# Kernel tuning notes

Hardware: AMD Instinct MI355X
Metric: run time of the kernel (lower is better)

The kernel has to match this reference:

```python
import jax, jax.numpy as jnp
import numpy as np

GAMMA = 2.0
EPS = 1e-12  # tf.nn.l2_normalize epsilon


def setup_inputs() -> dict:
    key = jax.random.key(0)
    k1, k2 = jax.random.split(key)
    B, H, W_, C = 8, 56, 56, 256
    x = jax.random.normal(k1, (B, H, W_, C), dtype=jnp.float32)
    W = jax.random.normal(k2, (C, C), dtype=jnp.float32) * 0.05
    return {"x": x, "W": W}


def reference(x, W):
    B, H, Wd, C = x.shape
    hw = H * Wd
    # transform branch: 1x1 conv, no bias (num_layers=1)
    t = jnp.einsum('bhwc,cd->bhwd', x, W).reshape(B, hw, C)
    # pixel affinity: cosine similarity (tf: -cosine_similarity == cos sim)
    xf = x.reshape(B, hw, C)
    inv_norm = jax.lax.rsqrt(jnp.maximum(jnp.sum(xf * xf, axis=-1, keepdims=True), EPS))
    xn = xf * inv_norm
    sim = jnp.einsum('bic,bjc->bij', xn, xn)  # [B, hw, hw]
    sim = jnp.power(jax.nn.relu(sim), GAMMA)
    y = jnp.einsum('bij,bjc->bic', sim, t)
    return y.reshape(B, H, Wd, C)
```

## Files before the change

kernel.cpp:

```cpp
#include <hip/hip_runtime.h>

#define HW 3136
#define CH 256
#define NJT 49
#define NIT 25
#define NPIX 25088

typedef __attribute__((ext_vector_type(8))) short bf16x8;
typedef __attribute__((ext_vector_type(4))) float f32x4;
typedef __attribute__((ext_vector_type(16))) float f32x16;
typedef unsigned short u16;
typedef unsigned int u32;

static __device__ __forceinline__ u16 f2bf(float f){
  union { float f; u32 u; } v; v.f = f;
  u32 r = v.u + 0x7FFFu + ((v.u >> 16) & 1u);
  return (u16)(r >> 16);
}

static __device__ __forceinline__ void gload16(const void* g, void* l){
  __builtin_amdgcn_global_load_lds(
      (const __attribute__((address_space(1))) unsigned int*)g,
      (__attribute__((address_space(3))) unsigned int*)l, 16, 0, 0);
}

static __device__ __forceinline__ f32x16 zero16(){
  f32x16 v;
  #pragma unroll
  for (int e = 0; e < 16; ++e) v[e] = 0.f;
  return v;
}

#define MFMA32(A,B,C) __builtin_amdgcn_mfma_f32_32x32x16_bf16((A),(B),(C),0,0,0)

__global__ __launch_bounds__(256) void prep_wt(const float* __restrict__ W,
                                               u16* __restrict__ Wt){
  const int o = blockIdx.x, i = threadIdx.x;
  Wt[o*CH + i] = f2bf(W[i*CH + o]);
}

__global__ __launch_bounds__(256) void gemm_t(const float* __restrict__ x,
                                              const u16* __restrict__ Wt,
                                              u16* __restrict__ xn_bf,
                                              u16* __restrict__ tT){
  __shared__ u16 sT[256*64];
  const int jt = blockIdx.x, b = blockIdx.y;
  const int tid = threadIdx.x, wid = tid >> 6, lane = tid & 63;
  const int l15 = lane & 15, l4 = lane >> 4;
  const int j0 = jt * 64;
  const int row = j0 + wid*16 + l15;
  const float* xp = x + ((size_t)b*HW + row)*CH + l4*8;

  float xv[8][8];
  float ss = 0.f;
  #pragma unroll
  for (int kb = 0; kb < 8; ++kb){
    const float4 v0 = *(const float4*)(xp + kb*32);
    const float4 v1 = *(const float4*)(xp + kb*32 + 4);
    xv[kb][0]=v0.x; xv[kb][1]=v0.y; xv[kb][2]=v0.z; xv[kb][3]=v0.w;
    xv[kb][4]=v1.x; xv[kb][5]=v1.y; xv[kb][6]=v1.z; xv[kb][7]=v1.w;
    #pragma unroll
    for (int e = 0; e < 8; ++e) ss += xv[kb][e]*xv[kb][e];
  }
  ss += __shfl_xor(ss, 16);
  ss += __shfl_xor(ss, 32);
  const float inv = rsqrtf(fmaxf(ss, 1e-12f));

  bf16x8 ax[8];
  #pragma unroll
  for (int kb = 0; kb < 8; ++kb){
    bf16x8 a, n;
    #pragma unroll
    for (int e = 0; e < 8; ++e){
      a[e] = (short)f2bf(xv[kb][e]);
      n[e] = (short)f2bf(xv[kb][e]*inv);
    }
    ax[kb] = a;
    *(bf16x8*)(xn_bf + ((size_t)b*HW + row)*CH + kb*32 + l4*8) = n;
  }

  f32x4 acc[16];
  #pragma unroll
  for (int n = 0; n < 16; ++n) acc[n] = f32x4{0.f,0.f,0.f,0.f};
  #pragma unroll
  for (int kb = 0; kb < 8; ++kb){
    #pragma unroll
    for (int n0 = 0; n0 < 16; ++n0){
      const bf16x8 bb = *(const bf16x8*)(Wt + (n0*16 + l15)*CH + kb*32 + l4*8);
      acc[n0] = __builtin_amdgcn_mfma_f32_16x16x32_bf16(ax[kb], bb, acc[n0], 0, 0, 0);
    }
  }
  #pragma unroll
  for (int n0 = 0; n0 < 16; ++n0){
    const int c = n0*16 + l15;
    const int jloc = wid*16 + l4*4;
    const int gj = jloc >> 3;
    ushort4 w4;
    w4.x = f2bf(acc[n0][0]); w4.y = f2bf(acc[n0][1]);
    w4.z = f2bf(acc[n0][2]); w4.w = f2bf(acc[n0][3]);
    *(ushort4*)&sT[c*64 + ((gj ^ (c & 7)) * 8) + (jloc & 7)] = w4;
  }
  __syncthreads();
  #pragma unroll
  for (int p = 0; p < 8; ++p){
    const int c = p*32 + (tid >> 3);
    const int q = tid & 7;
    const bf16x8 v = *(const bf16x8*)&sT[c*64 + ((q ^ (c & 7)) * 8)];
    *(bf16x8*)(tT + ((size_t)b*CH + c)*HW + j0 + q*8) = v;
  }
}

__global__ __launch_bounds__(512) void ppm_main(const u16* __restrict__ xn,
                                                const u16* __restrict__ tT,
                                                float* __restrict__ out){
  __shared__ u16 SM[73728];

  const int it = blockIdx.x, b = blockIdx.y;
  const int tid = threadIdx.x, wid = tid >> 6, lane = tid & 63;
  const int l31 = lane & 31, hi = lane >> 5;
  const int i0 = it * 128;
  const int wj = wid >> 2, wi = wid & 3;
  u16* sPB = SM + 65536;

  bf16x8 aq[16];
  {
    int irow = i0 + wi*32 + l31;
    if (irow >= HW) irow = HW - 1;
    const u16* p = xn + ((size_t)b*HW + irow)*CH + hi*8;
    #pragma unroll
    for (int ks = 0; ks < 16; ++ks) aq[ks] = *(const bf16x8*)(p + ks*16);
  }

  f32x16 accY[4];
  #pragma unroll
  for (int cb = 0; cb < 4; ++cb) accY[cb] = zero16();

  const size_t xbase = (size_t)b*HW;
  const size_t tbase = (size_t)b*CH;

  {
    u16* nXJ = SM;
    u16* nTJ = SM + 16384;
    #pragma unroll
    for (int q = 0; q < 4; ++q){
      const int m = q*512 + tid;
      { const int row = m >> 5, g = m & 31;
        gload16(xn + (xbase + row)*CH + ((g ^ (row & 7))*8), &nXJ[m*8]); }
      { const int c = m >> 3, g = m & 7;
        gload16(tT + (tbase + c)*HW + ((g ^ (c & 7))*8), &nTJ[m*8]); }
    }
    __syncthreads();
  }

  #pragma unroll 1
  for (int jt = 0; jt < NJT; ++jt){
    const int buf = jt & 1;
    u16* sXJ = SM + buf*32768;
    u16* sTJ = sXJ + 16384;

    if (jt + 1 < NJT){
      u16* nXJ = SM + (buf ^ 1)*32768;
      u16* nTJ = nXJ + 16384;
      const int j0n = (jt + 1)*64;
      #pragma unroll
      for (int q = 0; q < 4; ++q){
        const int m = q*512 + tid;
        { const int row = m >> 5, g = m & 31;
          gload16(xn + (xbase + j0n + row)*CH + ((g ^ (row & 7))*8), &nXJ[m*8]); }
        { const int c = m >> 3, g = m & 7;
          gload16(tT + (tbase + c)*HW + j0n + ((g ^ (c & 7))*8), &nTJ[m*8]); }
      }
    }

    f32x16 sa = zero16(), sb = zero16();
    const int rj = wj*32 + l31;
    const int rsw = rj & 7;
    const u16* xjrow = &sXJ[rj*256];
    __builtin_amdgcn_s_setprio(1);
    #pragma unroll
    for (int kb = 0; kb < 8; ++kb){
      const bf16x8 a0 = *(const bf16x8*)&xjrow[(((kb*4 + hi)     ^ rsw) * 8)];
      const bf16x8 a1 = *(const bf16x8*)&xjrow[(((kb*4 + 2 + hi) ^ rsw) * 8)];
      sa = MFMA32(a0, aq[2*kb],   sa);
      sb = MFMA32(a1, aq[2*kb+1], sb);
    }
    __builtin_amdgcn_s_setprio(0);

    float s0,s1,s2,s3,s4,s5,s6,s7,s8,s9,s10,s11,s12,s13,s14,s15;
#define SREL(d, r) { float v_ = sa[r] + sb[r]; v_ = fmaxf(v_, 0.f); d = v_ * v_; }
    SREL(s0,0) SREL(s1,1) SREL(s2,2) SREL(s3,3) SREL(s4,4) SREL(s5,5) SREL(s6,6) SREL(s7,7)
    SREL(s8,8) SREL(s9,9) SREL(s10,10) SREL(s11,11) SREL(s12,12) SREL(s13,13) SREL(s14,14) SREL(s15,15)
#undef SREL
    u32 w0,w1,w2,w3,w4,w5,w6,w7;
#define PK(d, a, c) asm("v_cvt_pk_bf16_f32 %0, %1, %2" : "=v"(d) : "v"(a), "v"(c));
    PK(w0, s0, s1)  PK(w1, s2, s3)  PK(w2, s4, s5)  PK(w3, s6, s7)
    PK(w4, s8, s9)  PK(w5, s10,s11) PK(w6, s12,s13) PK(w7, s14,s15)
#undef PK
    asm volatile("v_permlane32_swap_b32 %0, %1" : "+v"(w0), "+v"(w2));
    asm volatile("v_permlane32_swap_b32 %0, %1" : "+v"(w1), "+v"(w3));
    asm volatile("v_permlane32_swap_b32 %0, %1" : "+v"(w4), "+v"(w6));
    asm volatile("v_permlane32_swap_b32 %0, %1" : "+v"(w5), "+v"(w7));
    union { u32 u[4]; bf16x8 v; } fb0, fb1;
    fb0.u[0]=w0; fb0.u[1]=w1; fb0.u[2]=w2; fb0.u[3]=w3;
    fb1.u[0]=w4; fb1.u[1]=w5; fb1.u[2]=w6; fb1.u[3]=w7;

    *(bf16x8*)&sPB[(wi*4 + 2*wj + 0)*512 + lane*8] = fb0.v;
    *(bf16x8*)&sPB[(wi*4 + 2*wj + 1)*512 + lane*8] = fb1.v;
    __syncthreads();

    bf16x8 pb[4];
    #pragma unroll
    for (int ks = 0; ks < 4; ++ks)
      pb[ks] = *(const bf16x8*)&sPB[(wi*4 + ks)*512 + lane*8];

    __builtin_amdgcn_s_setprio(1);
    #pragma unroll
    for (int ks = 0; ks < 4; ++ks){
      #pragma unroll
      for (int cb = 0; cb < 4; ++cb){
        const int c = wj*128 + cb*32 + l31;
        const bf16x8 af = *(const bf16x8*)&sTJ[c*64 + (((ks*2 + hi) ^ (c & 7)) * 8)];
        accY[cb] = MFMA32(af, pb[ks], accY[cb]);
      }
    }
    __builtin_amdgcn_s_setprio(0);

    __syncthreads();
  }

  float* Yl = (float*)SM;
  {
    const int il = wi*32 + l31;
    const int isw = (il & 7) << 2;
    #pragma unroll
    for (int cb = 0; cb < 4; ++cb)
      #pragma unroll
      for (int r = 0; r < 16; ++r){
        const int c = wj*128 + cb*32 + (r & 3) + 8*(r >> 2) + 4*hi;
        Yl[il*256 + (c ^ isw)] = accY[cb][r];
      }
  }
  __syncthreads();
  {
    const int i3 = tid >> 2;
    const int cq = (tid & 3) * 64;
    const int sw3 = (i3 & 7) << 2;
    if (i0 + i3 < HW){
      float* orow = out + ((size_t)b*HW + i0 + i3)*CH;
      #pragma unroll
      for (int q = 0; q < 16; ++q){
        const int c = cq + q*4;
        const float4 v = *(const float4*)&Yl[i3*256 + (c ^ sw3)];
        *(float4*)&orow[c] = v;
      }
    }
  }
}

extern "C" void kernel_launch(void* const* d_in, const int* in_sizes, int n_in,
                              void* d_out, int out_size, void* d_ws, size_t ws_size,
                              hipStream_t stream){
  const float* x = (const float*)d_in[0];
  const float* W = (const float*)d_in[1];
  float* out = (float*)d_out;
  char* ws = (char*)d_ws;

  const size_t SZ = (size_t)NPIX * CH * sizeof(u16);
  u16* xn_bf = (u16*)(ws);
  u16* tT    = (u16*)(ws + SZ);
  u16* Wt    = (u16*)(ws + 2*SZ);

  prep_wt<<<CH, CH, 0, stream>>>(W, Wt);
  gemm_t<<<dim3(NJT, 8), 256, 0, stream>>>(x, Wt, xn_bf, tT);
  ppm_main<<<dim3(NIT, 8), 512, 0, stream>>>(xn_bf, tT, out);
}
```

Measured before the change: 149.8 us.

## Software-pipeline the P·T MFMA stage one tile behind the similarity stage

The loop is restructured so that the second GEMM (similarity tile times transformed features) for tile jt-1 runs in the same iteration as the first GEMM for tile jt. The X and T tile loads are split into separate double-buffered stages, and the P buffer is double-buffered too. This removes one __syncthreads per iteration and lets the two MFMA phases and the loads interleave. In exchange, LDS use grows from 144 KiB to 160 KiB per block, which leaves no LDS headroom, and a final drain PV step is added after the loop.

Result: no change. 150.3 us (+0.3%).

```diff
diff --git a/kernel.cpp b/kernel.cpp
--- a/kernel.cpp
+++ b/kernel.cpp
@@ -113,14 +113,13 @@
 __global__ __launch_bounds__(512) void ppm_main(const u16* __restrict__ xn,
                                                 const u16* __restrict__ tT,
                                                 float* __restrict__ out){
-  __shared__ u16 SM[73728];
+  __shared__ u16 SM[81920];
 
   const int it = blockIdx.x, b = blockIdx.y;
   const int tid = threadIdx.x, wid = tid >> 6, lane = tid & 63;
   const int l31 = lane & 31, hi = lane >> 5;
   const int i0 = it * 128;
   const int wj = wid >> 2, wi = wid & 3;
-  u16* sPB = SM + 65536;
 
   bf16x8 aq[16];
   {
@@ -138,44 +137,62 @@
   const size_t xbase = (size_t)b*HW;
   const size_t tbase = (size_t)b*CH;
 
-  {
-    u16* nXJ = SM;
-    u16* nTJ = SM + 16384;
+  auto STAGE_XN = [&](int jt){
+    u16* dst = SM + (jt & 1)*16384;
+    const int j0n = jt*64;
     #pragma unroll
     for (int q = 0; q < 4; ++q){
       const int m = q*512 + tid;
-      { const int row = m >> 5, g = m & 31;
-        gload16(xn + (xbase + row)*CH + ((g ^ (row & 7))*8), &nXJ[m*8]); }
-      { const int c = m >> 3, g = m & 7;
-        gload16(tT + (tbase + c)*HW + ((g ^ (c & 7))*8), &nTJ[m*8]); }
-    }
-    __syncthreads();
-  }
+      const int row = m >> 5, g = m & 31;
+      gload16(xn + (xbase + j0n + row)*CH + ((g ^ (row & 7))*8), &dst[m*8]);
+    }
+  };
+  auto STAGE_TT = [&](int jt){
+    u16* dst = SM + 32768 + (jt & 1)*16384;
+    const int j0n = jt*64;
+    #pragma unroll
+    for (int q = 0; q < 4; ++q){
+      const int m = q*512 + tid;
+      const int c = m >> 3, g = m & 7;
+      gload16(tT + (tbase + c)*HW + j0n + ((g ^ (c & 7))*8), &dst[m*8]);
+    }
+  };
+
+  auto PV = [&](int p){
+    const u16* sTJp = SM + 32768 + (p & 1)*16384;
+    const u16* sPBp = SM + 65536 + (p & 1)*8192;
+    bf16x8 pb[4];
+    #pragma unroll
+    for (int ks = 0; ks < 4; ++ks)
+      pb[ks] = *(const bf16x8*)&sPBp[(wi*4 + ks)*512 + lane*8];
+    __builtin_amdgcn_s_setprio(1);
+    #pragma unroll
+    for (int ks = 0; ks < 4; ++ks){
+      #pragma unroll
+      for (int cb = 0; cb < 4; ++cb){
+        const int c = wj*128 + cb*32 + l31;
+        const bf16x8 af = *(const bf16x8*)&sTJp[c*64 + (((ks*2 + hi) ^ (c & 7)) * 8)];
+        accY[cb] = MFMA32(af, pb[ks], accY[cb]);
+      }
+    }
+    __builtin_amdgcn_s_setprio(0);
+  };
+
+  STAGE_XN(0);
+  __syncthreads();
 
   #pragma unroll 1
   for (int jt = 0; jt < NJT; ++jt){
-    const int buf = jt & 1;
-    u16* sXJ = SM + buf*32768;
-    u16* sTJ = sXJ + 16384;
-
-    if (jt + 1 < NJT){
-      u16* nXJ = SM + (buf ^ 1)*32768;
-      u16* nTJ = nXJ + 16384;
-      const int j0n = (jt + 1)*64;
-      #pragma unroll
-      for (int q = 0; q < 4; ++q){
-        const int m = q*512 + tid;
-        { const int row = m >> 5, g = m & 31;
-          gload16(xn + (xbase + j0n + row)*CH + ((g ^ (row & 7))*8), &nXJ[m*8]); }
-        { const int c = m >> 3, g = m & 7;
-          gload16(tT + (tbase + c)*HW + j0n + ((g ^ (c & 7))*8), &nTJ[m*8]); }
-      }
-    }
-
+    if (jt + 1 < NJT) STAGE_XN(jt + 1);
+    STAGE_TT(jt);
+
+    if (jt > 0) PV(jt - 1);
+
+    const u16* sXJk = SM + (jt & 1)*16384;
     f32x16 sa = zero16(), sb = zero16();
     const int rj = wj*32 + l31;
     const int rsw = rj & 7;
-    const u16* xjrow = &sXJ[rj*256];
+    const u16* xjrow = &sXJk[rj*256];
     __builtin_amdgcn_s_setprio(1);
     #pragma unroll
     for (int kb = 0; kb < 8; ++kb){
@@ -204,29 +221,15 @@
     fb0.u[0]=w0; fb0.u[1]=w1; fb0.u[2]=w2; fb0.u[3]=w3;
     fb1.u[0]=w4; fb1.u[1]=w5; fb1.u[2]=w6; fb1.u[3]=w7;
 
-    *(bf16x8*)&sPB[(wi*4 + 2*wj + 0)*512 + lane*8] = fb0.v;
-    *(bf16x8*)&sPB[(wi*4 + 2*wj + 1)*512 + lane*8] = fb1.v;
+    u16* sPBk = SM + 65536 + (jt & 1)*8192;
+    *(bf16x8*)&sPBk[(wi*4 + 2*wj + 0)*512 + lane*8] = fb0.v;
+    *(bf16x8*)&sPBk[(wi*4 + 2*wj + 1)*512 + lane*8] = fb1.v;
+
     __syncthreads();
-
-    bf16x8 pb[4];
-    #pragma unroll
-    for (int ks = 0; ks < 4; ++ks)
-      pb[ks] = *(const bf16x8*)&sPB[(wi*4 + ks)*512 + lane*8];
-
-    __builtin_amdgcn_s_setprio(1);
-    #pragma unroll
-    for (int ks = 0; ks < 4; ++ks){
-      #pragma unroll
-      for (int cb = 0; cb < 4; ++cb){
-        const int c = wj*128 + cb*32 + l31;
-        const bf16x8 af = *(const bf16x8*)&sTJ[c*64 + (((ks*2 + hi) ^ (c & 7)) * 8)];
-        accY[cb] = MFMA32(af, pb[ks], accY[cb]);
-      }
-    }
-    __builtin_amdgcn_s_setprio(0);
-
-    __syncthreads();
-  }
+  }
+
+  PV(NJT - 1);
+  __syncthreads();
 
   float* Yl = (float*)SM;
   {
```
